# Optimization experiments

Measured on AMD Instinct MI355X. Metric: run time of the kernel, lower is better.

Reference implementation:

```python
import jax, jax.numpy as jnp
import numpy as np

DIM = 1024
HEADS = 8
NUM_KEYS = 256
TOPK = 32
D_HEAD = DIM // HEADS
BATCH = 2
SEQ = 2048


def setup_inputs() -> dict:
    key = jax.random.key(0)
    ks = jax.random.split(key, 5)
    x = jax.random.normal(ks[0], (BATCH, SEQ, DIM), jnp.float32)
    # nn.Linear(dim, 2*dim, bias=False): weight (2*dim, dim)
    Wq = jax.random.normal(ks[1], (2 * DIM, DIM), jnp.float32) * (DIM ** -0.5)
    # nn.Parameter(torch.randn(heads, num_keys, 2, d_head))
    keys = jax.random.normal(ks[2], (HEADS, NUM_KEYS, 2, D_HEAD), jnp.float32)
    # nn.Parameter(torch.randn(heads, num_keys**2, d_head))
    values = jax.random.normal(ks[3], (HEADS, NUM_KEYS ** 2, D_HEAD), jnp.float32)
    # nn.Linear(dim, dim): weight (dim, dim), bias (dim,)
    Wo = jax.random.normal(ks[4], (DIM, DIM), jnp.float32) * (DIM ** -0.5)
    bo = jnp.zeros((DIM,), jnp.float32)
    return {"x": x, "Wq": Wq, "keys": keys, "values": values, "Wo": Wo, "bo": bo}


def reference(x, Wq, keys, values, Wo, bo):
    b, t, e = x.shape
    h, dh, k, nk = HEADS, D_HEAD, TOPK, NUM_KEYS
    # to_queries + chunk(2, dim=-1) + stack -> (2, b, t, h, d_head)
    q = x @ Wq.T                                    # (b, t, 2*dim)
    q = q.reshape(b, t, 2, e).transpose(2, 0, 1, 3)  # (2, b, t, dim), matches chunk+stack
    q = q.reshape(2, b, t, h, dh)
    # dual sub-key scores: (b, h, t, 2, num_keys)
    dots = jnp.einsum('pbthd,hnpd->bhtpn', q, keys)
    # top-k over num_keys per sub-key
    scores, indices = jax.lax.top_k(dots, k)         # (b, h, t, 2, k)
    # faithful to source: chunk(2, dim=2) splits the TIME axis
    th = t // 2
    s0, s1 = scores[:, :, :th], scores[:, :, th:]
    i0, i1 = indices[:, :, :th], indices[:, :, th:]
    # Cartesian combination: (b, h, t//2, 2, k, k) -> (b, h, t, k*k)
    all_scores = (s0[..., :, None] + s1[..., None, :]).reshape(b, h, t, k * k)
    all_indices = (i0[..., :, None] * nk + i1[..., None, :]).reshape(b, h, t, k * k)
    # final top-k over the k^2 candidates
    final_scores, final_idx = jax.lax.top_k(all_scores, k)   # (b, h, t, k)
    value_indices = jnp.take_along_axis(all_indices, final_idx, axis=-1)  # (b, h, t, k)
    attn = jax.nn.softmax(final_scores, axis=-1)
    # gather values per head: values (h, nk^2, dh), idx (b, h, t, k) -> (b, h, t, k, dh)
    sel = jax.vmap(lambda v, idx: v[idx], in_axes=(0, 1), out_axes=1)(values, value_indices)
    out = jnp.einsum('bhtk,bhtkd->bhtd', attn, sel)  # weighted sum over top-k
    out = out.transpose(0, 2, 1, 3).reshape(b, t, e)
    return out @ Wo.T + bo
```

## Files before the change

kernel.cpp:

```cpp
#include <hip/hip_runtime.h>

typedef unsigned int u32;
typedef unsigned long long u64;
typedef _Float16 f16;
typedef __attribute__((ext_vector_type(4))) _Float16 f16x4;
typedef __attribute__((ext_vector_type(8))) _Float16 f16x8;
typedef __attribute__((ext_vector_type(4))) float f32x4;
typedef const __attribute__((address_space(1))) void* gp_t;
typedef __attribute__((address_space(3))) void* lp_t;

#define TSEQ 2048

__device__ __forceinline__ u32 f2sort(float f) {
  u32 u = __float_as_uint(f);
  return u ^ ((u32)((int)u >> 31) | 0x80000000u);
}
__device__ __forceinline__ float sort2f(u32 u) {
  u ^= (u & 0x80000000u) ? 0x80000000u : 0xFFFFFFFFu;
  return __uint_as_float(u);
}

__device__ __forceinline__ void glds16(const f16* g, f16* l) {
  __builtin_amdgcn_global_load_lds((gp_t)g, (lp_t)l, 16, 0, 0);
}

__device__ __forceinline__ u32 umax2(u32 a, u32 b) { return a > b ? a : b; }

__device__ __forceinline__ u32 dppmax16(u32 v) {
  u32 t;
  t = (u32)__builtin_amdgcn_update_dpp(0, (int)v, 0x128, 0xF, 0xF, true);
  v = v > t ? v : t;
  t = (u32)__builtin_amdgcn_update_dpp(0, (int)v, 0x124, 0xF, 0xF, true);
  v = v > t ? v : t;
  t = (u32)__builtin_amdgcn_update_dpp(0, (int)v, 0x122, 0xF, 0xF, true);
  v = v > t ? v : t;
  t = (u32)__builtin_amdgcn_update_dpp(0, (int)v, 0x121, 0xF, 0xF, true);
  v = v > t ? v : t;
  return v;
}
__device__ __forceinline__ float dppsum16(float v) {
  float t;
  t = __int_as_float(
      __builtin_amdgcn_update_dpp(0, __float_as_int(v), 0x128, 0xF, 0xF, true));
  v += t;
  t = __int_as_float(
      __builtin_amdgcn_update_dpp(0, __float_as_int(v), 0x124, 0xF, 0xF, true));
  v += t;
  t = __int_as_float(
      __builtin_amdgcn_update_dpp(0, __float_as_int(v), 0x122, 0xF, 0xF, true));
  v += t;
  t = __int_as_float(
      __builtin_amdgcn_update_dpp(0, __float_as_int(v), 0x121, 0xF, 0xF, true));
  v += t;
  return v;
}

__global__ __launch_bounds__(256) void cvt_all(
    const float* __restrict__ x, const float* __restrict__ wq,
    const float* __restrict__ wo, const float* __restrict__ ky,
    f16* __restrict__ xd, f16* __restrict__ wqd, f16* __restrict__ wod,
    f16* __restrict__ kyd) {
  int g = blockIdx.x * 256 + threadIdx.x;
  const float* s;
  f16* d;
  int off;
  if (g < 1048576)      { s = x;  d = xd;  off = g; }
  else if (g < 1572864) { s = wq; d = wqd; off = g - 1048576; }
  else if (g < 1835008) { s = wo; d = wod; off = g - 1572864; }
  else                  { s = ky; d = kyd; off = g - 1835008; }
  float4 v = ((const float4*)s)[off];
  f16x4 o;
  o[0] = (f16)v.x; o[1] = (f16)v.y; o[2] = (f16)v.z; o[3] = (f16)v.w;
  ((f16x4*)d)[off] = o;
}

__global__ __launch_bounds__(256) void gemm_f16(
    const f16* __restrict__ A, int lda, const f16* __restrict__ B, int ldb,
    const float* __restrict__ bias, void* __restrict__ Cv, int ldc, int K,
    int c_f16) {
  __shared__ f16 As[128 * 32];
  __shared__ f16 Bs[128 * 32];
  const int tid = threadIdx.x;
  const int lane = tid & 63, wave = tid >> 6;
  const int m0 = blockIdx.y << 7, n0 = blockIdx.x << 7;
  const int c0 = wave * 128 + lane, c1 = c0 + 64;
  const int r0 = c0 >> 2, s0 = c0 & 3;
  const int r1 = c1 >> 2, s1 = c1 & 3;
  const f16* Ab = A + (size_t)m0 * lda;
  const f16* Bb = B + (size_t)n0 * ldb;
  const int fm = lane & 15, fq = lane >> 4, fk = fq << 3;
  const int wm = (wave >> 1) << 6, wn = (wave & 1) << 6;
  f32x4 acc[4][4] = {};
  for (int k0 = 0; k0 < K; k0 += 32) {
    __syncthreads();
    glds16(Ab + (size_t)r0 * lda + k0 + s0 * 8, As + (size_t)c0 * 8 - lane * 8);
    glds16(Ab + (size_t)r1 * lda + k0 + s1 * 8, As + (size_t)c1 * 8 - lane * 8);
    glds16(Bb + (size_t)r0 * ldb + k0 + s0 * 8, Bs + (size_t)c0 * 8 - lane * 8);
    glds16(Bb + (size_t)r1 * ldb + k0 + s1 * 8, Bs + (size_t)c1 * 8 - lane * 8);
    __syncthreads();
    f16x8 af[4], bf[4];
#pragma unroll
    for (int mi = 0; mi < 4; mi++)
      af[mi] = *(const f16x8*)&As[(wm + mi * 16 + fm) * 32 + fk];
#pragma unroll
    for (int nj = 0; nj < 4; nj++)
      bf[nj] = *(const f16x8*)&Bs[(wn + nj * 16 + fm) * 32 + fk];
#pragma unroll
    for (int mi = 0; mi < 4; mi++)
#pragma unroll
      for (int nj = 0; nj < 4; nj++)
        acc[mi][nj] = __builtin_amdgcn_mfma_f32_16x16x32_f16(
            af[mi], bf[nj], acc[mi][nj], 0, 0, 0);
  }
  if (c_f16) {
    f16* C = (f16*)Cv;
#pragma unroll
    for (int mi = 0; mi < 4; mi++)
#pragma unroll
      for (int r = 0; r < 4; r++) {
        int row = m0 + wm + mi * 16 + fq * 4 + r;
        f16* cp = C + (size_t)row * ldc + n0 + wn + fm;
#pragma unroll
        for (int nj = 0; nj < 4; nj++) cp[nj * 16] = (f16)acc[mi][nj][r];
      }
  } else {
    float* C = (float*)Cv;
    float bb[4];
#pragma unroll
    for (int nj = 0; nj < 4; nj++)
      bb[nj] = bias ? bias[n0 + wn + nj * 16 + fm] : 0.f;
#pragma unroll
    for (int mi = 0; mi < 4; mi++)
#pragma unroll
      for (int r = 0; r < 4; r++) {
        int row = m0 + wm + mi * 16 + fq * 4 + r;
        float* cp = C + (size_t)row * ldc + n0 + wn + fm;
#pragma unroll
        for (int nj = 0; nj < 4; nj++) cp[nj * 16] = acc[mi][nj][r] + bb[nj];
      }
  }
}

__global__ __launch_bounds__(256) void dots_topk1(
    const f16* __restrict__ Q,
    const f16* __restrict__ keysf,
    float* __restrict__ s1s, int* __restrict__ s1i) {
  __shared__ f16 As[64 * 32];
  __shared__ f16 Bs[256 * 32];
  const int tid = threadIdx.x;
  const int lane = tid & 63, wave = tid >> 6;
  const int z = blockIdx.x;
  const int h = z >> 1, p = z & 1;
  const int m0 = blockIdx.y << 6;
  const f16* Aq = Q + (size_t)m0 * 2048 + p * 1024 + h * 128;
  const f16* Bk = keysf + ((size_t)h * 512 + p) * 128;
  const int cA = wave * 64 + lane;
  const int rA = cA >> 2, sA = cA & 3;
  const int fm = lane & 15, fq = lane >> 4, fk = fq << 3;
  f32x4 acc[16] = {};
  for (int k0 = 0; k0 < 128; k0 += 32) {
    __syncthreads();
    glds16(Aq + (size_t)rA * 2048 + k0 + sA * 8, As + (size_t)cA * 8 - lane * 8);
#pragma unroll
    for (int c = 0; c < 4; c++) {
      int cB = (wave * 4 + c) * 64 + lane;
      int rB = cB >> 2, sB = cB & 3;
      glds16(Bk + (size_t)rB * 256 + k0 + sB * 8,
             Bs + (size_t)cB * 8 - lane * 8);
    }
    __syncthreads();
    f16x8 af = *(const f16x8*)&As[(wave * 16 + fm) * 32 + fk];
#pragma unroll
    for (int j = 0; j < 16; j++) {
      f16x8 bf = *(const f16x8*)&Bs[(j * 16 + fm) * 32 + fk];
      acc[j] = __builtin_amdgcn_mfma_f32_16x16x32_f16(af, bf, acc[j], 0, 0, 0);
    }
  }
  for (int r = 0; r < 4; r++) {
    u32 key[16];
#pragma unroll
    for (int j = 0; j < 16; j++)
      key[j] = (f2sort(acc[j][r]) & ~0xFFu) | (u32)((j << 4) | fm);
    u32 g0 = 0, g1 = 0;
    for (int it = 0; it < 32; it++) {
      u32 t0 = umax2(key[0], key[1]), t1 = umax2(key[2], key[3]);
      u32 t2 = umax2(key[4], key[5]), t3 = umax2(key[6], key[7]);
      u32 t4 = umax2(key[8], key[9]), t5 = umax2(key[10], key[11]);
      u32 t6 = umax2(key[12], key[13]), t7 = umax2(key[14], key[15]);
      t0 = umax2(t0, t1); t2 = umax2(t2, t3);
      t4 = umax2(t4, t5); t6 = umax2(t6, t7);
      u32 lm = umax2(umax2(t0, t2), umax2(t4, t6));
      u32 gm = dppmax16(lm);
#pragma unroll
      for (int j = 0; j < 16; j++) key[j] = (key[j] == gm) ? 0u : key[j];
      bool sel = (fm == (it & 15));
      if (it < 16) g0 = sel ? gm : g0;
      else         g1 = sel ? gm : g1;
    }
    int m = m0 + wave * 16 + (fq << 2) + r;
    int b = m >> 11, t = m & 2047;
    size_t orow = ((((size_t)(b * 8 + h)) * TSEQ + t) * 2 + p) * 32;
    s1s[orow + fm] = sort2f(g0 & ~0xFFu);
    s1s[orow + fm + 16] = sort2f(g1 & ~0xFFu);
    s1i[orow + fm] = (int)(g0 & 0xFFu);
    s1i[orow + fm + 16] = (int)(g1 & 0xFFu);
  }
}

__global__ __launch_bounds__(256) void topk2_gather(
    const float* __restrict__ s1s, const int* __restrict__ s1i,
    const float* __restrict__ valf, f16* __restrict__ headout) {
  __shared__ unsigned short cand[128];
  __shared__ float s0sh[16][32];
  __shared__ float s1sh[16][32];
  __shared__ int i0sh[16][32];
  __shared__ int i1sh[16][32];
  __shared__ int vtab[16][32];
  __shared__ float wtab[16][32];
  const int tid = threadIdx.x;
  if (tid < 128) {
    int c = tid;
    unsigned short enc = 0xFFFF;
    if (c < 119) {
      int rem = c, i = 0;
      for (i = 0; i < 32; i++) {
        int cnt = 32 / (i + 1);
        if (rem < cnt) break;
        rem -= cnt;
      }
      enc = (unsigned short)((i << 5) | rem);
    }
    cand[tid] = enc;
  }
  const int rloc = tid >> 4;
  const int l = tid & 15;
  const int row = blockIdx.x * 16 + rloc;
  const int b = row >> 14;
  const int h = (row >> 11) & 7;
  const int t = row & 2047;
  const int tt = t >> 1, p = t & 1;
  size_t rbase = (size_t)(b * 8 + h) * TSEQ;
  size_t base0 = ((rbase + tt) * 2 + p) * 32;
  size_t base1 = ((rbase + tt + 1024) * 2 + p) * 32;
  s0sh[rloc][l] = s1s[base0 + l];
  s0sh[rloc][l + 16] = s1s[base0 + l + 16];
  s1sh[rloc][l] = s1s[base1 + l];
  s1sh[rloc][l + 16] = s1s[base1 + l + 16];
  i0sh[rloc][l] = s1i[base0 + l];
  i0sh[rloc][l + 16] = s1i[base0 + l + 16];
  i1sh[rloc][l] = s1i[base1 + l];
  i1sh[rloc][l + 16] = s1i[base1 + l + 16];
  __syncthreads();
  u32 key[8];
#pragma unroll
  for (int s = 0; s < 8; s++) {
    int c = l + 16 * s;
    unsigned short e = cand[c];
    u32 kk = 0u;
    if (e != 0xFFFF) {
      float v = s0sh[rloc][e >> 5] + s1sh[rloc][e & 31];
      kk = (f2sort(v) & ~0xFFu) | (u32)c;
    }
    key[s] = kk;
  }
  u32 g0 = 0, g1 = 0;
  for (int it = 0; it < 32; it++) {
    u32 t0 = umax2(key[0], key[1]), t1 = umax2(key[2], key[3]);
    u32 t2 = umax2(key[4], key[5]), t3 = umax2(key[6], key[7]);
    u32 lm = umax2(umax2(t0, t1), umax2(t2, t3));
    u32 gm = dppmax16(lm);
#pragma unroll
    for (int s = 0; s < 8; s++) key[s] = (key[s] == gm) ? 0u : key[s];
    bool sel = (l == (it & 15));
    if (it < 16) g0 = sel ? gm : g0;
    else         g1 = sel ? gm : g1;
  }
  float sc0 = sort2f(g0 & ~0xFFu);
  float sc1 = sort2f(g1 & ~0xFFu);
  unsigned short e0c = cand[g0 & 0xFFu];
  unsigned short e1c = cand[g1 & 0xFFu];
  int vidx0 = i0sh[rloc][e0c >> 5] * 256 + i1sh[rloc][e0c & 31];
  int vidx1 = i0sh[rloc][e1c >> 5] * 256 + i1sh[rloc][e1c & 31];
  float mx = __int_as_float(
      __builtin_amdgcn_ds_swizzle(__float_as_int(sc0), 0x010));
  float e0 = __expf(sc0 - mx);
  float e1 = __expf(sc1 - mx);
  float inv = 1.0f / dppsum16(e0 + e1);
  vtab[rloc][l] = vidx0;
  vtab[rloc][l + 16] = vidx1;
  wtab[rloc][l] = e0 * inv;
  wtab[rloc][l + 16] = e1 * inv;
  const float* vb = valf + (((size_t)h) << 23) + (size_t)l * 8;
  float accf[8] = {};
#pragma unroll 8
  for (int k = 0; k < 32; k++) {
    int vi = vtab[rloc][k];
    float wk = wtab[rloc][k];
    const float4* vp = (const float4*)(vb + (size_t)vi * 128);
    float4 v0 = vp[0];
    float4 v1 = vp[1];
    accf[0] += wk * v0.x; accf[1] += wk * v0.y;
    accf[2] += wk * v0.z; accf[3] += wk * v0.w;
    accf[4] += wk * v1.x; accf[5] += wk * v1.y;
    accf[6] += wk * v1.z; accf[7] += wk * v1.w;
  }
  f16x8 o;
#pragma unroll
  for (int j = 0; j < 8; j++) o[j] = (f16)accf[j];
  f16* op = headout + (size_t)(b * TSEQ + t) * 1024 + h * 128 + l * 8;
  *(f16x8*)op = o;
}

extern "C" void kernel_launch(void* const* d_in, const int* in_sizes, int n_in,
                              void* d_out, int out_size, void* d_ws,
                              size_t ws_size, hipStream_t stream) {
  const float* x    = (const float*)d_in[0];
  const float* Wq   = (const float*)d_in[1];
  const float* keys = (const float*)d_in[2];
  const float* vals = (const float*)d_in[3];
  const float* Wo   = (const float*)d_in[4];
  const float* bo   = (const float*)d_in[5];
  float* out = (float*)d_out;
  char* ws = (char*)d_ws;
  f16*   xf   = (f16*)(ws);
  f16*   wqf  = (f16*)(ws + (size_t)(8u << 20));
  f16*   wof  = (f16*)(ws + (size_t)(12u << 20));
  f16*   kyf  = (f16*)(ws + (size_t)(14u << 20));
  f16*   Qf   = (f16*)(ws + (size_t)(16u << 20));
  float* s1s  = (float*)(ws + (size_t)(32u << 20));
  int*   s1i  = (int*)(ws + (size_t)(40u << 20));
  f16*   hof  = (f16*)(ws + (size_t)(48u << 20));

  cvt_all<<<dim3(7680), 256, 0, stream>>>(x, Wq, Wo, keys, xf, wqf, wof, kyf);
  gemm_f16<<<dim3(16, 32), 256, 0, stream>>>(xf, 1024, wqf, 1024, nullptr, Qf,
                                             2048, 1024, 1);
  dots_topk1<<<dim3(16, 64), 256, 0, stream>>>(Qf, kyf, s1s, s1i);
  topk2_gather<<<dim3(32768 / 16), 256, 0, stream>>>(s1s, s1i, vals, hof);
  gemm_f16<<<dim3(8, 32), 256, 0, stream>>>(hof, 1024, wof, 1024, bo, out,
                                            1024, 1024, 0);
}
```

Measured before the change: 530.8 us.

## Interleave top-k row selection, persist gather blocks, narrow output GEMM tile

In the first top-k kernel, each wave now runs the iterative max-extraction for two rows at once, so the two independent DPP reduction chains can overlap and hide latency. The top-k2/gather kernel becomes a persistent loop of 512 blocks, each handling 4 row groups. This amortises building the candidate table, at the cost of fewer resident blocks to hide the latency of the random value gathers. The output GEMM is templated to a 128x64 tile, doubling its grid to 512 blocks for better CU occupancy, with less reuse per block as the tradeoff.

After: 535.6 us. About the same (+0.9%).

```diff
diff --git a/kernel.cpp b/kernel.cpp
--- a/kernel.cpp
+++ b/kernel.cpp
@@ -53,6 +53,16 @@
       __builtin_amdgcn_update_dpp(0, __float_as_int(v), 0x121, 0xF, 0xF, true));
   v += t;
   return v;
+}
+
+__device__ __forceinline__ u32 tree16(const u32* k) {
+  u32 t0 = umax2(k[0], k[1]), t1 = umax2(k[2], k[3]);
+  u32 t2 = umax2(k[4], k[5]), t3 = umax2(k[6], k[7]);
+  u32 t4 = umax2(k[8], k[9]), t5 = umax2(k[10], k[11]);
+  u32 t6 = umax2(k[12], k[13]), t7 = umax2(k[14], k[15]);
+  t0 = umax2(t0, t1); t2 = umax2(t2, t3);
+  t4 = umax2(t4, t5); t6 = umax2(t6, t7);
+  return umax2(umax2(t0, t2), umax2(t4, t6));
 }
 
 __global__ __launch_bounds__(256) void cvt_all(
@@ -74,41 +84,52 @@
   ((f16x4*)d)[off] = o;
 }
 
+template <int BN>
 __global__ __launch_bounds__(256) void gemm_f16(
     const f16* __restrict__ A, int lda, const f16* __restrict__ B, int ldb,
     const float* __restrict__ bias, void* __restrict__ Cv, int ldc, int K,
     int c_f16) {
+  constexpr int NJ = BN / 32;
   __shared__ f16 As[128 * 32];
-  __shared__ f16 Bs[128 * 32];
+  __shared__ f16 Bs[BN * 32];
   const int tid = threadIdx.x;
   const int lane = tid & 63, wave = tid >> 6;
-  const int m0 = blockIdx.y << 7, n0 = blockIdx.x << 7;
+  const int m0 = blockIdx.y << 7, n0 = blockIdx.x * BN;
   const int c0 = wave * 128 + lane, c1 = c0 + 64;
   const int r0 = c0 >> 2, s0 = c0 & 3;
   const int r1 = c1 >> 2, s1 = c1 & 3;
+  const int cB = wave * 64 + lane;
+  const int rB = cB >> 2, sB = cB & 3;
   const f16* Ab = A + (size_t)m0 * lda;
   const f16* Bb = B + (size_t)n0 * ldb;
   const int fm = lane & 15, fq = lane >> 4, fk = fq << 3;
-  const int wm = (wave >> 1) << 6, wn = (wave & 1) << 6;
-  f32x4 acc[4][4] = {};
+  const int wm = (wave >> 1) << 6, wn = (wave & 1) * (BN / 2);
+  f32x4 acc[4][NJ] = {};
   for (int k0 = 0; k0 < K; k0 += 32) {
     __syncthreads();
     glds16(Ab + (size_t)r0 * lda + k0 + s0 * 8, As + (size_t)c0 * 8 - lane * 8);
     glds16(Ab + (size_t)r1 * lda + k0 + s1 * 8, As + (size_t)c1 * 8 - lane * 8);
-    glds16(Bb + (size_t)r0 * ldb + k0 + s0 * 8, Bs + (size_t)c0 * 8 - lane * 8);
-    glds16(Bb + (size_t)r1 * ldb + k0 + s1 * 8, Bs + (size_t)c1 * 8 - lane * 8);
+    if constexpr (BN == 128) {
+      glds16(Bb + (size_t)r0 * ldb + k0 + s0 * 8,
+             Bs + (size_t)c0 * 8 - lane * 8);
+      glds16(Bb + (size_t)r1 * ldb + k0 + s1 * 8,
+             Bs + (size_t)c1 * 8 - lane * 8);
+    } else {
+      glds16(Bb + (size_t)rB * ldb + k0 + sB * 8,
+             Bs + (size_t)cB * 8 - lane * 8);
+    }
     __syncthreads();
-    f16x8 af[4], bf[4];
+    f16x8 af[4], bf[NJ];
 #pragma unroll
     for (int mi = 0; mi < 4; mi++)
       af[mi] = *(const f16x8*)&As[(wm + mi * 16 + fm) * 32 + fk];
 #pragma unroll
-    for (int nj = 0; nj < 4; nj++)
+    for (int nj = 0; nj < NJ; nj++)
       bf[nj] = *(const f16x8*)&Bs[(wn + nj * 16 + fm) * 32 + fk];
 #pragma unroll
     for (int mi = 0; mi < 4; mi++)
 #pragma unroll
-      for (int nj = 0; nj < 4; nj++)
+      for (int nj = 0; nj < NJ; nj++)
         acc[mi][nj] = __builtin_amdgcn_mfma_f32_16x16x32_f16(
             af[mi], bf[nj], acc[mi][nj], 0, 0, 0);
   }
@@ -121,13 +142,13 @@
         int row = m0 + wm + mi * 16 + fq * 4 + r;
         f16* cp = C + (size_t)row * ldc + n0 + wn + fm;
 #pragma unroll
-        for (int nj = 0; nj < 4; nj++) cp[nj * 16] = (f16)acc[mi][nj][r];
+        for (int nj = 0; nj < NJ; nj++) cp[nj * 16] = (f16)acc[mi][nj][r];
       }
   } else {
     float* C = (float*)Cv;
-    float bb[4];
-#pragma unroll
-    for (int nj = 0; nj < 4; nj++)
+    float bb[NJ];
+#pragma unroll
+    for (int nj = 0; nj < NJ; nj++)
       bb[nj] = bias ? bias[n0 + wn + nj * 16 + fm] : 0.f;
 #pragma unroll
     for (int mi = 0; mi < 4; mi++)
@@ -136,7 +157,7 @@
         int row = m0 + wm + mi * 16 + fq * 4 + r;
         float* cp = C + (size_t)row * ldc + n0 + wn + fm;
 #pragma unroll
-        for (int nj = 0; nj < 4; nj++) cp[nj * 16] = acc[mi][nj][r] + bb[nj];
+        for (int nj = 0; nj < NJ; nj++) cp[nj * 16] = acc[mi][nj][r] + bb[nj];
       }
   }
 }
@@ -176,34 +197,48 @@
       acc[j] = __builtin_amdgcn_mfma_f32_16x16x32_f16(af, bf, acc[j], 0, 0, 0);
     }
   }
-  for (int r = 0; r < 4; r++) {
-    u32 key[16];
-#pragma unroll
-    for (int j = 0; j < 16; j++)
-      key[j] = (f2sort(acc[j][r]) & ~0xFFu) | (u32)((j << 4) | fm);
-    u32 g0 = 0, g1 = 0;
+#pragma unroll
+  for (int rp = 0; rp < 2; rp++) {
+    u32 keyA[16], keyB[16];
+#pragma unroll
+    for (int j = 0; j < 16; j++) {
+      keyA[j] = (f2sort(acc[j][2 * rp]) & ~0xFFu) | (u32)((j << 4) | fm);
+      keyB[j] = (f2sort(acc[j][2 * rp + 1]) & ~0xFFu) | (u32)((j << 4) | fm);
+    }
+    u32 g0A = 0, g1A = 0, g0B = 0, g1B = 0;
     for (int it = 0; it < 32; it++) {
-      u32 t0 = umax2(key[0], key[1]), t1 = umax2(key[2], key[3]);
-      u32 t2 = umax2(key[4], key[5]), t3 = umax2(key[6], key[7]);
-      u32 t4 = umax2(key[8], key[9]), t5 = umax2(key[10], key[11]);
-      u32 t6 = umax2(key[12], key[13]), t7 = umax2(key[14], key[15]);
-      t0 = umax2(t0, t1); t2 = umax2(t2, t3);
-      t4 = umax2(t4, t5); t6 = umax2(t6, t7);
-      u32 lm = umax2(umax2(t0, t2), umax2(t4, t6));
-      u32 gm = dppmax16(lm);
-#pragma unroll
-      for (int j = 0; j < 16; j++) key[j] = (key[j] == gm) ? 0u : key[j];
+      u32 lmA = tree16(keyA);
+      u32 lmB = tree16(keyB);
+      u32 gmA = dppmax16(lmA);
+      u32 gmB = dppmax16(lmB);
+#pragma unroll
+      for (int j = 0; j < 16; j++) {
+        keyA[j] = (keyA[j] == gmA) ? 0u : keyA[j];
+        keyB[j] = (keyB[j] == gmB) ? 0u : keyB[j];
+      }
       bool sel = (fm == (it & 15));
-      if (it < 16) g0 = sel ? gm : g0;
-      else         g1 = sel ? gm : g1;
-    }
-    int m = m0 + wave * 16 + (fq << 2) + r;
-    int b = m >> 11, t = m & 2047;
-    size_t orow = ((((size_t)(b * 8 + h)) * TSEQ + t) * 2 + p) * 32;
-    s1s[orow + fm] = sort2f(g0 & ~0xFFu);
-    s1s[orow + fm + 16] = sort2f(g1 & ~0xFFu);
-    s1i[orow + fm] = (int)(g0 & 0xFFu);
-    s1i[orow + fm + 16] = (int)(g1 & 0xFFu);
+      if (it < 16) {
+        g0A = sel ? gmA : g0A;
+        g0B = sel ? gmB : g0B;
+      } else {
+        g1A = sel ? gmA : g1A;
+        g1B = sel ? gmB : g1B;
+      }
+    }
+    int mA = m0 + wave * 16 + (fq << 2) + 2 * rp;
+    int bA = mA >> 11, tA = mA & 2047;
+    size_t orowA = ((((size_t)(bA * 8 + h)) * TSEQ + tA) * 2 + p) * 32;
+    s1s[orowA + fm] = sort2f(g0A & ~0xFFu);
+    s1s[orowA + fm + 16] = sort2f(g1A & ~0xFFu);
+    s1i[orowA + fm] = (int)(g0A & 0xFFu);
+    s1i[orowA + fm + 16] = (int)(g1A & 0xFFu);
+    int mB = mA + 1;
+    int bB = mB >> 11, tB = mB & 2047;
+    size_t orowB = ((((size_t)(bB * 8 + h)) * TSEQ + tB) * 2 + p) * 32;
+    s1s[orowB + fm] = sort2f(g0B & ~0xFFu);
+    s1s[orowB + fm + 16] = sort2f(g1B & ~0xFFu);
+    s1i[orowB + fm] = (int)(g0B & 0xFFu);
+    s1i[orowB + fm + 16] = (int)(g1B & 0xFFu);
   }
 }
 
@@ -232,83 +267,86 @@
     }
     cand[tid] = enc;
   }
+  __syncthreads();
   const int rloc = tid >> 4;
   const int l = tid & 15;
-  const int row = blockIdx.x * 16 + rloc;
-  const int b = row >> 14;
-  const int h = (row >> 11) & 7;
-  const int t = row & 2047;
-  const int tt = t >> 1, p = t & 1;
-  size_t rbase = (size_t)(b * 8 + h) * TSEQ;
-  size_t base0 = ((rbase + tt) * 2 + p) * 32;
-  size_t base1 = ((rbase + tt + 1024) * 2 + p) * 32;
-  s0sh[rloc][l] = s1s[base0 + l];
-  s0sh[rloc][l + 16] = s1s[base0 + l + 16];
-  s1sh[rloc][l] = s1s[base1 + l];
-  s1sh[rloc][l + 16] = s1s[base1 + l + 16];
-  i0sh[rloc][l] = s1i[base0 + l];
-  i0sh[rloc][l + 16] = s1i[base0 + l + 16];
-  i1sh[rloc][l] = s1i[base1 + l];
-  i1sh[rloc][l + 16] = s1i[base1 + l + 16];
-  __syncthreads();
-  u32 key[8];
-#pragma unroll
-  for (int s = 0; s < 8; s++) {
-    int c = l + 16 * s;
-    unsigned short e = cand[c];
-    u32 kk = 0u;
-    if (e != 0xFFFF) {
-      float v = s0sh[rloc][e >> 5] + s1sh[rloc][e & 31];
-      kk = (f2sort(v) & ~0xFFu) | (u32)c;
-    }
-    key[s] = kk;
-  }
-  u32 g0 = 0, g1 = 0;
-  for (int it = 0; it < 32; it++) {
-    u32 t0 = umax2(key[0], key[1]), t1 = umax2(key[2], key[3]);
-    u32 t2 = umax2(key[4], key[5]), t3 = umax2(key[6], key[7]);
-    u32 lm = umax2(umax2(t0, t1), umax2(t2, t3));
-    u32 gm = dppmax16(lm);
-#pragma unroll
-    for (int s = 0; s < 8; s++) key[s] = (key[s] == gm) ? 0u : key[s];
-    bool sel = (l == (it & 15));
-    if (it < 16) g0 = sel ? gm : g0;
-    else         g1 = sel ? gm : g1;
-  }
-  float sc0 = sort2f(g0 & ~0xFFu);
-  float sc1 = sort2f(g1 & ~0xFFu);
-  unsigned short e0c = cand[g0 & 0xFFu];
-  unsigned short e1c = cand[g1 & 0xFFu];
-  int vidx0 = i0sh[rloc][e0c >> 5] * 256 + i1sh[rloc][e0c & 31];
-  int vidx1 = i0sh[rloc][e1c >> 5] * 256 + i1sh[rloc][e1c & 31];
-  float mx = __int_as_float(
-      __builtin_amdgcn_ds_swizzle(__float_as_int(sc0), 0x010));
-  float e0 = __expf(sc0 - mx);
-  float e1 = __expf(sc1 - mx);
-  float inv = 1.0f / dppsum16(e0 + e1);
-  vtab[rloc][l] = vidx0;
-  vtab[rloc][l + 16] = vidx1;
-  wtab[rloc][l] = e0 * inv;
-  wtab[rloc][l + 16] = e1 * inv;
-  const float* vb = valf + (((size_t)h) << 23) + (size_t)l * 8;
-  float accf[8] = {};
+  for (int g = 0; g < 4; g++) {
+    const int grp = g * 512 + blockIdx.x;
+    const int row = grp * 16 + rloc;
+    const int b = row >> 14;
+    const int h = (row >> 11) & 7;
+    const int t = row & 2047;
+    const int tt = t >> 1, p = t & 1;
+    size_t rbase = (size_t)(b * 8 + h) * TSEQ;
+    size_t base0 = ((rbase + tt) * 2 + p) * 32;
+    size_t base1 = ((rbase + tt + 1024) * 2 + p) * 32;
+    s0sh[rloc][l] = s1s[base0 + l];
+    s0sh[rloc][l + 16] = s1s[base0 + l + 16];
+    s1sh[rloc][l] = s1s[base1 + l];
+    s1sh[rloc][l + 16] = s1s[base1 + l + 16];
+    i0sh[rloc][l] = s1i[base0 + l];
+    i0sh[rloc][l + 16] = s1i[base0 + l + 16];
+    i1sh[rloc][l] = s1i[base1 + l];
+    i1sh[rloc][l + 16] = s1i[base1 + l + 16];
+    u32 key[8];
+#pragma unroll
+    for (int s = 0; s < 8; s++) {
+      int c = l + 16 * s;
+      unsigned short e = cand[c];
+      u32 kk = 0u;
+      if (e != 0xFFFF) {
+        float v = s0sh[rloc][e >> 5] + s1sh[rloc][e & 31];
+        kk = (f2sort(v) & ~0xFFu) | (u32)c;
+      }
+      key[s] = kk;
+    }
+    u32 g0 = 0, g1 = 0;
+    for (int it = 0; it < 32; it++) {
+      u32 t0 = umax2(key[0], key[1]), t1 = umax2(key[2], key[3]);
+      u32 t2 = umax2(key[4], key[5]), t3 = umax2(key[6], key[7]);
+      u32 lm = umax2(umax2(t0, t1), umax2(t2, t3));
+      u32 gm = dppmax16(lm);
+#pragma unroll
+      for (int s = 0; s < 8; s++) key[s] = (key[s] == gm) ? 0u : key[s];
+      bool sel = (l == (it & 15));
+      if (it < 16) g0 = sel ? gm : g0;
+      else         g1 = sel ? gm : g1;
+    }
+    float sc0 = sort2f(g0 & ~0xFFu);
+    float sc1 = sort2f(g1 & ~0xFFu);
+    unsigned short e0c = cand[g0 & 0xFFu];
+    unsigned short e1c = cand[g1 & 0xFFu];
+    int vidx0 = i0sh[rloc][e0c >> 5] * 256 + i1sh[rloc][e0c & 31];
+    int vidx1 = i0sh[rloc][e1c >> 5] * 256 + i1sh[rloc][e1c & 31];
+    float mx = __int_as_float(
+        __builtin_amdgcn_ds_swizzle(__float_as_int(sc0), 0x010));
+    float e0 = __expf(sc0 - mx);
+    float e1 = __expf(sc1 - mx);
+    float inv = 1.0f / dppsum16(e0 + e1);
+    vtab[rloc][l] = vidx0;
+    vtab[rloc][l + 16] = vidx1;
+    wtab[rloc][l] = e0 * inv;
+    wtab[rloc][l + 16] = e1 * inv;
+    const float* vb = valf + (((size_t)h) << 23) + (size_t)l * 8;
+    float accf[8] = {};
 #pragma unroll 8
-  for (int k = 0; k < 32; k++) {
-    int vi = vtab[rloc][k];
-    float wk = wtab[rloc][k];
-    const float4* vp = (const float4*)(vb + (size_t)vi * 128);
-    float4 v0 = vp[0];
-    float4 v1 = vp[1];
-    accf[0] += wk * v0.x; accf[1] += wk * v0.y;
-    accf[2] += wk * v0.z; accf[3] += wk * v0.w;
-    accf[4] += wk * v1.x; accf[5] += wk * v1.y;
-    accf[6] += wk * v1.z; accf[7] += wk * v1.w;
-  }
-  f16x8 o;
-#pragma unroll
-  for (int j = 0; j < 8; j++) o[j] = (f16)accf[j];
-  f16* op = headout + (size_t)(b * TSEQ + t) * 1024 + h * 128 + l * 8;
-  *(f16x8*)op = o;
+    for (int k = 0; k < 32; k++) {
+      int vi = vtab[rloc][k];
+      float wk = wtab[rloc][k];
+      const float4* vp = (const float4*)(vb + (size_t)vi * 128);
+      float4 v0 = vp[0];
+      float4 v1 = vp[1];
+      accf[0] += wk * v0.x; accf[1] += wk * v0.y;
+      accf[2] += wk * v0.z; accf[3] += wk * v0.w;
+      accf[4] += wk * v1.x; accf[5] += wk * v1.y;
+      accf[6] += wk * v1.z; accf[7] += wk * v1.w;
+    }
+    f16x8 o;
+#pragma unroll
+    for (int j = 0; j < 8; j++) o[j] = (f16)accf[j];
+    f16* op = headout + (size_t)(b * TSEQ + t) * 1024 + h * 128 + l * 8;
+    *(f16x8*)op = o;
+  }
 }
 
 extern "C" void kernel_launch(void* const* d_in, const int* in_sizes, int n_in,
@@ -332,10 +370,10 @@
   f16*   hof  = (f16*)(ws + (size_t)(48u << 20));
 
   cvt_all<<<dim3(7680), 256, 0, stream>>>(x, Wq, Wo, keys, xf, wqf, wof, kyf);
-  gemm_f16<<<dim3(16, 32), 256, 0, stream>>>(xf, 1024, wqf, 1024, nullptr, Qf,
-                                             2048, 1024, 1);
+  gemm_f16<128><<<dim3(16, 32), 256, 0, stream>>>(xf, 1024, wqf, 1024, nullptr,
+                                                  Qf, 2048, 1024, 1);
   dots_topk1<<<dim3(16, 64), 256, 0, stream>>>(Qf, kyf, s1s, s1i);
-  topk2_gather<<<dim3(32768 / 16), 256, 0, stream>>>(s1s, s1i, vals, hof);
-  gemm_f16<<<dim3(8, 32), 256, 0, stream>>>(hof, 1024, wof, 1024, bo, out,
-                                            1024, 1024, 0);
-}
+  topk2_gather<<<dim3(512), 256, 0, stream>>>(s1s, s1i, vals, hof);
+  gemm_f16<64><<<dim3(16, 32), 256, 0, stream>>>(hof, 1024, wof, 1024, bo, out,
+                                                 1024, 1024, 0);
+}
```
